# Performance work log

Hardware: AMD Instinct MI355X
Metric: run time of the kernel (lower is better)

The kernel has to match this reference:

```python
import jax, jax.numpy as jnp
import numpy as np

BASE = 257
HASH_MOD = 4096
WINDOWS = (2, 4, 8, 16)
MATCH_OFFSETS = (1, 2, 4, 8)
CHUNK = 32
EPS_LN = 1e-5


def _shift_right(x, k):
    # (B,T) -> shifted right by k along time, zero-filled
    B, T = x.shape
    return jnp.concatenate([jnp.zeros((B, k), x.dtype), x[:, :T - k]], axis=1)


def _rolling_hashes(chars):
    # polynomial rolling hash over each window size, mod HASH_MOD -> (B,T,S) int32
    c = chars.astype(jnp.int32)
    hs = []
    for w in WINDOWS:
        acc = jnp.zeros_like(c)
        p = 1
        for j in range(w):  # small fixed loop (<=16)
            acc = acc + _shift_right(c, j) * p
            p = (p * BASE) % HASH_MOD
        hs.append(acc % HASH_MOD)
    return jnp.stack(hs, axis=2)


def _match_features(chars):
    feats = []
    for k in MATCH_OFFSETS:
        m = (chars == _shift_right(chars, k)).astype(jnp.float32)
        m = m.at[:, :k].set(0.0)
        feats.append(m)
    return jnp.stack(feats, axis=-1)  # (B,T,n_match)


def _layer_norm(x, g, b):
    mu = jnp.mean(x, axis=-1, keepdims=True)
    var = jnp.mean((x - mu) ** 2, axis=-1, keepdims=True)
    return (x - mu) * jax.lax.rsqrt(var + EPS_LN) * g + b


def _forward(chars, emb_byte, hash_tables, Wq, bq, conv_w, conv_b, Win, b_in,
             Wg, bg, Wi, bi, Wo, bo, ln_g, ln_b, mlp_w, mlp_b, Wout, bout):
    B, T = chars.shape
    byte_emb = emb_byte[chars]                       # (B,T,Eb)
    hidx = _rolling_hashes(chars)                    # (B,T,S)
    scale_embeds = jnp.stack(
        [hash_tables[s][hidx[:, :, s]] for s in range(len(WINDOWS))], axis=2
    )                                                # (B,T,S,E)
    # scale attention: query from byte embedding, softmax over scales
    E = scale_embeds.shape[-1]
    q = byte_emb @ Wq + bq                           # (B,T,E)
    scores = jnp.einsum('bte,btse->bts', q, scale_embeds) / jnp.sqrt(jnp.float32(E))
    w = jax.nn.softmax(scores, axis=-1)
    hash_feat = jnp.einsum('bts,btse->bte', w, scale_embeds)
    # causal depthwise conv + silu
    C = hash_feat.shape[-1]
    kk = conv_w.shape[-1]
    ht = jnp.moveaxis(hash_feat, 1, 2)               # (B,C,T)
    ht = jnp.pad(ht, ((0, 0), (0, 0), (kk - 1, 0)))
    ht = jax.lax.conv_general_dilated(
        ht, conv_w, window_strides=(1,), padding='VALID',
        dimension_numbers=('NCH', 'OIH', 'NCH'), feature_group_count=C)
    hash_feat = jax.nn.silu(jnp.moveaxis(ht + conv_b[None, :, None], 2, 1))
    mf = _match_features(chars)
    feat = jnp.concatenate([byte_emb, hash_feat, mf], axis=-1)
    h = jax.nn.silu(feat @ Win + b_in)               # (B,T,H)
    # TinyScan: chunked log-space gated scan, carry across chunks via lax.scan
    gates = jax.nn.sigmoid(h @ Wg + bg)              # (B,T,S)
    drive = (1.0 - gates) * (h @ Wi + bi)
    S = gates.shape[-1]
    nC = T // CHUNK
    g = gates.reshape(B, nC, CHUNK, S).transpose(1, 0, 2, 3)
    d = drive.reshape(B, nC, CHUNK, S).transpose(1, 0, 2, 3)

    def step(hc, ab):
        a, b = ab                                    # (B,K,S)
        log_a = jnp.log(jnp.maximum(a, 1e-6))
        cum_a = jnp.exp(jnp.cumsum(log_a, axis=1))
        inv = 1.0 / jnp.maximum(cum_a, 1e-8)
        cum_wb = jnp.cumsum(b * inv, axis=1)
        out = cum_a * (hc[:, None, :] + cum_wb)
        return out[:, -1], out

    _, states = jax.lax.scan(step, jnp.zeros((B, S), h.dtype), (g, d))
    states = states.transpose(1, 0, 2, 3).reshape(B, T, S)
    h = _layer_norm(h + states @ Wo + bo, ln_g, ln_b)
    # residual MLP blocks: x + silu(Linear(x))
    for l in range(mlp_w.shape[0]):
        h = h + jax.nn.silu(h @ mlp_w[l] + mlp_b[l])
    return h @ Wout + bout                           # (B,T,V)


def setup_inputs() -> dict:
    key = jax.random.key(0)
    ks = jax.random.split(key, 12)
    B, T, V = 8, 8192, 256
    EB, E, H, SS, KC, NM, NR = 64, 64, 512, 32, 4, 4, 3
    feat = EB + E + NM

    def lin(k, i, o):
        return (jax.random.normal(k, (i, o), jnp.float32) / np.sqrt(i)).astype(jnp.float32)

    return {
        'chars': jax.random.randint(ks[0], (B, T), 0, V),
        'emb_byte': jax.random.normal(ks[1], (V, EB), jnp.float32) * 0.02,
        'hash_tables': jax.random.normal(ks[2], (len(WINDOWS), HASH_MOD, E), jnp.float32) * 0.02,
        'Wq': lin(ks[3], EB, E), 'bq': jnp.zeros((E,), jnp.float32),
        'conv_w': jax.random.normal(ks[4], (E, 1, KC), jnp.float32) * 0.2,
        'conv_b': jnp.zeros((E,), jnp.float32),
        'Win': lin(ks[5], feat, H), 'b_in': jnp.zeros((H,), jnp.float32),
        'Wg': lin(ks[6], H, SS), 'bg': jnp.zeros((SS,), jnp.float32),
        'Wi': lin(ks[7], H, SS), 'bi': jnp.zeros((SS,), jnp.float32),
        'Wo': lin(ks[8], SS, H), 'bo': jnp.zeros((H,), jnp.float32),
        'ln_g': jnp.ones((H,), jnp.float32), 'ln_b': jnp.zeros((H,), jnp.float32),
        'mlp_w': jax.random.normal(ks[9], (NR, H, H), jnp.float32) / np.sqrt(H),
        'mlp_b': jnp.zeros((NR, H), jnp.float32),
        'Wout': lin(ks[10], H, V), 'bout': jnp.zeros((V,), jnp.float32),
    }


def reference(chars, emb_byte, hash_tables, Wq, bq, conv_w, conv_b, Win, b_in,
              Wg, bg, Wi, bi, Wo, bo, ln_g, ln_b, mlp_w, mlp_b, Wout, bout):
    return _forward(chars, emb_byte, hash_tables, Wq, bq, conv_w, conv_b, Win, b_in,
                    Wg, bg, Wi, bi, Wo, bo, ln_g, ln_b, mlp_w, mlp_b, Wout, bout)
```

## Files before the change

kernel.cpp:

```cpp
#include <hip/hip_runtime.h>
#include <hip/hip_bf16.h>
#include <math.h>

#define B_ 8
#define T_ 8192
#define V_ 256
#define EB_ 64
#define E_ 64
#define H_ 512
#define SS_ 32
#define FEATP_ 160
#define NCH_ 256
#define CHUNK_ 32

typedef __attribute__((ext_vector_type(8))) short bf8;
typedef __attribute__((ext_vector_type(16))) float accv;

#define AS1(p) (__attribute__((address_space(1))) void*)(void*)(p)
#define AS3(p) (__attribute__((address_space(3))) void*)(void*)(p)

__device__ __forceinline__ float silu_f(float x) { return x / (1.0f + expf(-x)); }
__device__ __forceinline__ float sigm_f(float x) { return 1.0f / (1.0f + expf(-x)); }
__device__ __forceinline__ float bf2f(__hip_bfloat16 v) { return __bfloat162float(v); }
__device__ __forceinline__ __hip_bfloat16 f2bf(float v) { return __float2bfloat16(v); }
__device__ __forceinline__ float us2f(ushort u) {
    union { float f; unsigned int u32; } c; c.u32 = ((unsigned int)u) << 16; return c.f;
}
__device__ __forceinline__ ushort f2us(float v) {
    __hip_bfloat16 t = __float2bfloat16(v);
    return *reinterpret_cast<ushort*>(&t);
}

template <int KD>
__device__ __forceinline__ void mm128(const __hip_bfloat16* __restrict__ A,
                                      const __hip_bfloat16* __restrict__ Wt,
                                      int m0, int n0, accv (&acc)[2][2]) {
    __shared__ __align__(16) ushort lA[128 * 32];
    __shared__ __align__(16) ushort lB[128 * 32];
    int tid = threadIdx.x;
    int lane = tid & 63, w = tid >> 6;
    int wm = w & 1, wn = w >> 1;
    int c0 = w * 128 + lane;
    int c1 = c0 + 64;
    const ushort* Ab = (const ushort*)A;
    const ushort* Bb = (const ushort*)Wt;
    const ushort* gA0 = Ab + (size_t)(m0 + (c0 >> 2)) * KD + (c0 & 3) * 8;
    const ushort* gA1 = Ab + (size_t)(m0 + (c1 >> 2)) * KD + (c1 & 3) * 8;
    const ushort* gB0 = Bb + (size_t)(n0 + (c0 >> 2)) * KD + (c0 & 3) * 8;
    const ushort* gB1 = Bb + (size_t)(n0 + (c1 >> 2)) * KD + (c1 & 3) * 8;
    ushort* dA0 = &lA[(w * 128) * 8];
    ushort* dA1 = &lA[(w * 128 + 64) * 8];
    ushort* dB0 = &lB[(w * 128) * 8];
    ushort* dB1 = &lB[(w * 128 + 64) * 8];
    const ushort* pa = &lA[(64 * wm + (lane & 31)) * 32 + (lane >> 5) * 8];
    const ushort* pb = &lB[(64 * wn + (lane & 31)) * 32 + (lane >> 5) * 8];

    for (int kt = 0; kt < KD; kt += 32) {
        __builtin_amdgcn_global_load_lds(AS1(gA0 + kt), AS3(dA0), 16, 0, 0);
        __builtin_amdgcn_global_load_lds(AS1(gA1 + kt), AS3(dA1), 16, 0, 0);
        __builtin_amdgcn_global_load_lds(AS1(gB0 + kt), AS3(dB0), 16, 0, 0);
        __builtin_amdgcn_global_load_lds(AS1(gB1 + kt), AS3(dB1), 16, 0, 0);
        __syncthreads();
#pragma unroll
        for (int ks = 0; ks < 2; ks++) {
            bf8 a0 = *(const bf8*)(pa + ks * 16);
            bf8 a1 = *(const bf8*)(pa + 32 * 32 + ks * 16);
            bf8 b0 = *(const bf8*)(pb + ks * 16);
            bf8 b1 = *(const bf8*)(pb + 32 * 32 + ks * 16);
            acc[0][0] = __builtin_amdgcn_mfma_f32_32x32x16_bf16(a0, b0, acc[0][0], 0, 0, 0);
            acc[0][1] = __builtin_amdgcn_mfma_f32_32x32x16_bf16(a0, b1, acc[0][1], 0, 0, 0);
            acc[1][0] = __builtin_amdgcn_mfma_f32_32x32x16_bf16(a1, b0, acc[1][0], 0, 0, 0);
            acc[1][1] = __builtin_amdgcn_mfma_f32_32x32x16_bf16(a1, b1, acc[1][1], 0, 0, 0);
        }
        __syncthreads();
    }
}

__device__ __forceinline__ void zero_acc(accv (&acc)[2][2]) {
#pragma unroll
    for (int i = 0; i < 2; i++)
#pragma unroll
        for (int j = 0; j < 2; j++)
#pragma unroll
            for (int r = 0; r < 16; r++) acc[i][j][r] = 0.0f;
}

#define CD_ROW(r, lane) (((r) & 3) + 8 * ((r) >> 2) + 4 * ((lane) >> 5))

__global__ __launch_bounds__(256) void k_mlp_mfma(const __hip_bfloat16* __restrict__ hin,
                                                  const __hip_bfloat16* __restrict__ Wt,
                                                  const float* __restrict__ bias,
                                                  __hip_bfloat16* __restrict__ hout) {
    accv acc[2][2];
    zero_acc(acc);
    int lane = threadIdx.x & 63, w = threadIdx.x >> 6, wm = w & 1, wn = w >> 1;
    int m0 = blockIdx.x * 128, n0 = blockIdx.y * 128;
    mm128<H_>(hin, Wt, m0, n0, acc);
#pragma unroll
    for (int i = 0; i < 2; i++)
#pragma unroll
        for (int j = 0; j < 2; j++) {
            int col = n0 + 64 * wn + 32 * j + (lane & 31);
            float bv = bias[col];
#pragma unroll
            for (int r = 0; r < 16; r++) {
                int row = m0 + 64 * wm + 32 * i + CD_ROW(r, lane);
                float v = acc[i][j][r] + bv;
                float res = bf2f(hin[(size_t)row * H_ + col]);
                hout[(size_t)row * H_ + col] = f2bf(res + silu_f(v));
            }
        }
}

__global__ __launch_bounds__(256) void k_win_mfma(const __hip_bfloat16* __restrict__ featb,
                                                  const __hip_bfloat16* __restrict__ Wt,
                                                  const float* __restrict__ bias,
                                                  __hip_bfloat16* __restrict__ hb) {
    accv acc[2][2];
    zero_acc(acc);
    int lane = threadIdx.x & 63, w = threadIdx.x >> 6, wm = w & 1, wn = w >> 1;
    int m0 = blockIdx.x * 128, n0 = blockIdx.y * 128;
    mm128<FEATP_>(featb, Wt, m0, n0, acc);
#pragma unroll
    for (int i = 0; i < 2; i++)
#pragma unroll
        for (int j = 0; j < 2; j++) {
            int col = n0 + 64 * wn + 32 * j + (lane & 31);
            float bv = bias[col];
#pragma unroll
            for (int r = 0; r < 16; r++) {
                int row = m0 + 64 * wm + 32 * i + CD_ROW(r, lane);
                hb[(size_t)row * H_ + col] = f2bf(silu_f(acc[i][j][r] + bv));
            }
        }
}

__global__ __launch_bounds__(256) void k_womm(const __hip_bfloat16* __restrict__ states_bf,
                                              const __hip_bfloat16* __restrict__ Wt_wo,
                                              const float* __restrict__ bo,
                                              const __hip_bfloat16* __restrict__ hb,
                                              __hip_bfloat16* __restrict__ tmp) {
    accv acc[2][2];
    zero_acc(acc);
    int lane = threadIdx.x & 63, w = threadIdx.x >> 6, wm = w & 1, wn = w >> 1;
    int m0 = blockIdx.x * 128, n0 = blockIdx.y * 128;
    mm128<SS_>(states_bf, Wt_wo, m0, n0, acc);
#pragma unroll
    for (int i = 0; i < 2; i++)
#pragma unroll
        for (int j = 0; j < 2; j++) {
            int col = n0 + 64 * wn + 32 * j + (lane & 31);
            float bv = bo[col];
#pragma unroll
            for (int r = 0; r < 16; r++) {
                int row = m0 + 64 * wm + 32 * i + CD_ROW(r, lane);
                float res = bf2f(hb[(size_t)row * H_ + col]);
                tmp[(size_t)row * H_ + col] = f2bf(res + acc[i][j][r] + bv);
            }
        }
}

__global__ __launch_bounds__(256) void k_ln(const __hip_bfloat16* __restrict__ tmp,
                                            const float* __restrict__ ln_g,
                                            const float* __restrict__ ln_b,
                                            __hip_bfloat16* __restrict__ hb) {
    int wave = threadIdx.x >> 6, lane = threadIdx.x & 63;
    int token = blockIdx.x * 4 + wave;
    const ushort* row = (const ushort*)(tmp + (size_t)token * H_) + lane * 8;
    bf8 xv = *(const bf8*)row;
    float x[8];
    float sm = 0.f, sq = 0.f;
#pragma unroll
    for (int i = 0; i < 8; i++) {
        x[i] = us2f((ushort)xv[i]);
        sm += x[i];
        sq += x[i] * x[i];
    }
#pragma unroll
    for (int off = 32; off; off >>= 1) {
        sm += __shfl_xor(sm, off, 64);
        sq += __shfl_xor(sq, off, 64);
    }
    float mu = sm * (1.0f / 512.0f);
    float var = sq * (1.0f / 512.0f) - mu * mu;
    float rstd = rsqrtf(fmaxf(var, 0.0f) + 1e-5f);
    float4 g0 = *(const float4*)(ln_g + lane * 8);
    float4 g1 = *(const float4*)(ln_g + lane * 8 + 4);
    float4 b0 = *(const float4*)(ln_b + lane * 8);
    float4 b1 = *(const float4*)(ln_b + lane * 8 + 4);
    float gg[8] = {g0.x, g0.y, g0.z, g0.w, g1.x, g1.y, g1.z, g1.w};
    float bb[8] = {b0.x, b0.y, b0.z, b0.w, b1.x, b1.y, b1.z, b1.w};
    bf8 o;
#pragma unroll
    for (int i = 0; i < 8; i++) o[i] = (short)f2us((x[i] - mu) * rstd * gg[i] + bb[i]);
    *(bf8*)((ushort*)(hb + (size_t)token * H_) + lane * 8) = o;
}

__global__ __launch_bounds__(256) void k_out_mfma(const __hip_bfloat16* __restrict__ hb,
                                                  const __hip_bfloat16* __restrict__ Wt,
                                                  const float* __restrict__ bout,
                                                  float* __restrict__ out) {
    accv acc[2][2];
    zero_acc(acc);
    int lane = threadIdx.x & 63, w = threadIdx.x >> 6, wm = w & 1, wn = w >> 1;
    int m0 = blockIdx.x * 128, n0 = blockIdx.y * 128;
    mm128<H_>(hb, Wt, m0, n0, acc);
#pragma unroll
    for (int i = 0; i < 2; i++)
#pragma unroll
        for (int j = 0; j < 2; j++) {
            int col = n0 + 64 * wn + 32 * j + (lane & 31);
            float bv = bout[col];
#pragma unroll
            for (int r = 0; r < 16; r++) {
                int row = m0 + 64 * wm + 32 * i + CD_ROW(r, lane);
                out[(size_t)row * V_ + col] = acc[i][j][r] + bv;
            }
        }
}

__global__ __launch_bounds__(256) void k_gates_mfma(const __hip_bfloat16* __restrict__ hb,
                                                    const __hip_bfloat16* __restrict__ Wt_gd,
                                                    const float* __restrict__ bg,
                                                    const float* __restrict__ bi,
                                                    float* __restrict__ gates,
                                                    float* __restrict__ drive) {
    __shared__ __align__(16) ushort lA[256 * 32];
    __shared__ __align__(16) ushort lB[64 * 32];
    int tid = threadIdx.x, lane = tid & 63, w = tid >> 6;
    int m0 = blockIdx.x * 256;
    accv acc[2][2];
    zero_acc(acc);
    const ushort* Ab = (const ushort*)hb;
    const ushort* Bb = (const ushort*)Wt_gd;
    const ushort* pa = &lA[(64 * w + (lane & 31)) * 32 + (lane >> 5) * 8];
    const ushort* pb = &lB[((lane & 31)) * 32 + (lane >> 5) * 8];
    int cb = w * 64 + lane;
    const ushort* gB = Bb + (size_t)(cb >> 2) * H_ + (cb & 3) * 8;
    for (int kt = 0; kt < H_; kt += 32) {
#pragma unroll
        for (int j = 0; j < 4; j++) {
            int c = w * 256 + j * 64 + lane;
            __builtin_amdgcn_global_load_lds(
                AS1(Ab + (size_t)(m0 + (c >> 2)) * H_ + (c & 3) * 8 + kt),
                AS3(&lA[(w * 256 + j * 64) * 8]), 16, 0, 0);
        }
        __builtin_amdgcn_global_load_lds(AS1(gB + kt), AS3(&lB[(w * 64) * 8]), 16, 0, 0);
        __syncthreads();
#pragma unroll
        for (int ks = 0; ks < 2; ks++) {
            bf8 a0 = *(const bf8*)(pa + ks * 16);
            bf8 a1 = *(const bf8*)(pa + 32 * 32 + ks * 16);
            bf8 b0 = *(const bf8*)(pb + ks * 16);
            bf8 b1 = *(const bf8*)(pb + 32 * 32 + ks * 16);
            acc[0][0] = __builtin_amdgcn_mfma_f32_32x32x16_bf16(a0, b0, acc[0][0], 0, 0, 0);
            acc[0][1] = __builtin_amdgcn_mfma_f32_32x32x16_bf16(a0, b1, acc[0][1], 0, 0, 0);
            acc[1][0] = __builtin_amdgcn_mfma_f32_32x32x16_bf16(a1, b0, acc[1][0], 0, 0, 0);
            acc[1][1] = __builtin_amdgcn_mfma_f32_32x32x16_bf16(a1, b1, acc[1][1], 0, 0, 0);
        }
        __syncthreads();
    }
    int c = lane & 31;
    float bgv = bg[c], biv = bi[c];
#pragma unroll
    for (int i = 0; i < 2; i++)
#pragma unroll
        for (int r = 0; r < 16; r++) {
            int row = m0 + 64 * w + 32 * i + CD_ROW(r, lane);
            float g = sigm_f(acc[i][0][r] + bgv);
            float d = (1.0f - g) * (acc[i][1][r] + biv);
            gates[(size_t)row * SS_ + c] = g;
            drive[(size_t)row * SS_ + c] = d;
        }
}

__global__ __launch_bounds__(256) void k_prep_w(const float* __restrict__ mlp_w,
                                                const float* __restrict__ Wout,
                                                const float* __restrict__ Win,
                                                const float* __restrict__ Wg,
                                                const float* __restrict__ Wi,
                                                const float* __restrict__ Wo,
                                                const float* __restrict__ Wq,
                                                const float* __restrict__ bq,
                                                const float* __restrict__ emb_byte,
                                                __hip_bfloat16* __restrict__ Wt_mlp,
                                                __hip_bfloat16* __restrict__ Wt_out,
                                                __hip_bfloat16* __restrict__ Wt_win,
                                                __hip_bfloat16* __restrict__ Wt_gd,
                                                __hip_bfloat16* __restrict__ Wt_wo,
                                                float* __restrict__ Qtab) {
    int idx = blockIdx.x * 256 + threadIdx.x;
    if (idx < 786432) {
        int l = idx >> 18, rem = idx & 262143;
        int n = rem >> 9, k = rem & 511;
        Wt_mlp[idx] = f2bf(mlp_w[l * 262144 + k * 512 + n]);
    } else if (idx < 786432 + 131072) {
        int rem = idx - 786432;
        int n = rem >> 9, k = rem & 511;
        Wt_out[rem] = f2bf(Wout[k * 256 + n]);
    } else if (idx < 786432 + 131072 + 81920) {
        int rem = idx - (786432 + 131072);
        int n = rem / 160, k = rem % 160;
        Wt_win[rem] = f2bf(k < 132 ? Win[k * 512 + n] : 0.0f);
    } else if (idx < 786432 + 131072 + 81920 + 32768) {
        int rem = idx - (786432 + 131072 + 81920);
        int n = rem >> 9, k = rem & 511;
        Wt_gd[rem] = f2bf(n < 32 ? Wg[k * 32 + n] : Wi[k * 32 + (n - 32)]);
    } else if (idx < 786432 + 131072 + 81920 + 32768 + 16384) {
        int rem = idx - (786432 + 131072 + 81920 + 32768);
        int n = rem >> 5, k = rem & 31;
        Wt_wo[rem] = f2bf(Wo[k * H_ + n]);
    } else if (idx < 786432 + 131072 + 81920 + 32768 + 16384 + 16384) {
        int rem = idx - (786432 + 131072 + 81920 + 32768 + 16384);
        int c = rem >> 6, e = rem & 63;
        float a = bq[e];
#pragma unroll 8
        for (int k = 0; k < 64; k++) a += emb_byte[c * 64 + k] * Wq[k * 64 + e];
        Qtab[rem] = a * 0.125f;
    }
}

__global__ __launch_bounds__(256) void k_token_feats(
    const int* __restrict__ chars, const float* __restrict__ emb_byte,
    const float* __restrict__ hash_tables, const float* __restrict__ Qtab,
    __hip_bfloat16* __restrict__ featb, float* __restrict__ hfpre) {
    int wave = threadIdx.x >> 6, lane = threadIdx.x & 63;
    int token = blockIdx.x * 4 + wave;
    int t = token & (T_ - 1);
    int b = token >> 13;
    const int* crow = chars + b * T_;
    int cv[16];
#pragma unroll
    for (int j = 0; j < 16; j++) cv[j] = (t >= j) ? crow[t - j] : 0;
    int acc = 0;
    int hidx[4];
#pragma unroll
    for (int j = 0; j < 16; j++) {
        acc += cv[j] * (1 + 256 * j);
        if (j == 1) hidx[0] = acc & 4095;
        if (j == 3) hidx[1] = acc & 4095;
        if (j == 7) hidx[2] = acc & 4095;
        if (j == 15) hidx[3] = acc & 4095;
    }
    int c0 = cv[0];
    float be = emb_byte[c0 * EB_ + lane];
    float q = Qtab[c0 * 64 + lane];
    float se[4];
#pragma unroll
    for (int s = 0; s < 4; s++) se[s] = hash_tables[(s * 4096 + hidx[s]) * E_ + lane];
    float sc[4];
#pragma unroll
    for (int s = 0; s < 4; s++) {
        float v = q * se[s];
#pragma unroll
        for (int off = 32; off; off >>= 1) v += __shfl_xor(v, off, 64);
        sc[s] = v;
    }
    float mx = fmaxf(fmaxf(sc[0], sc[1]), fmaxf(sc[2], sc[3]));
    float w0 = expf(sc[0] - mx), w1 = expf(sc[1] - mx), w2 = expf(sc[2] - mx), w3 = expf(sc[3] - mx);
    float inv = 1.0f / (w0 + w1 + w2 + w3);
    float hf = (w0 * se[0] + w1 * se[1] + w2 * se[2] + w3 * se[3]) * inv;
    featb[(size_t)token * FEATP_ + lane] = f2bf(be);
    hfpre[(size_t)token * E_ + lane] = hf;
    if (lane < 32) {
        float m = 0.0f;
        if (lane < 4) {
            int k = 1 << lane;
            m = (t >= k && c0 == cv[k]) ? 1.0f : 0.0f;
        }
        featb[(size_t)token * FEATP_ + 128 + lane] = f2bf(m);
    }
}

__global__ __launch_bounds__(256) void k_conv(
    const float* __restrict__ hfpre, const float* __restrict__ conv_w,
    const float* __restrict__ conv_b, __hip_bfloat16* __restrict__ featb) {
    int idx = blockIdx.x * 256 + threadIdx.x;
    int e = idx & 63;
    int bt = idx >> 6;
    int t = bt & (T_ - 1);
    float acc = conv_b[e];
#pragma unroll
    for (int k = 0; k < 4; k++) {
        int tt = t - 3 + k;
        if (tt >= 0) acc += hfpre[(size_t)(bt - 3 + k) * E_ + e] * conv_w[e * 4 + k];
    }
    featb[(size_t)bt * FEATP_ + 64 + e] = f2bf(silu_f(acc));
}

__global__ __launch_bounds__(256) void k_chunk_ab(
    const float* __restrict__ gates, const float* __restrict__ drive,
    float* __restrict__ chA, float* __restrict__ chB) {
    int gid = blockIdx.x * 256 + threadIdx.x;
    int s = gid & 31;
    int n = (gid >> 5) & (NCH_ - 1);
    int b = gid >> 13;
    int base = (b * T_ + n * CHUNK_) * SS_ + s;
    float suml = 0.f, cum_wb = 0.f, cum_a = 1.f;
    for (int i = 0; i < CHUNK_; i++) {
        float g = gates[base + i * SS_];
        float d = drive[base + i * SS_];
        suml += logf(fmaxf(g, 1e-6f));
        cum_a = expf(suml);
        cum_wb += d / fmaxf(cum_a, 1e-8f);
    }
    chA[gid] = cum_a;
    chB[gid] = cum_a * cum_wb;
}

__global__ void k_chunk_scan(const float* __restrict__ chA, const float* __restrict__ chB,
                             float* __restrict__ chH) {
    int tid = threadIdx.x;
    int b = tid >> 5, s = tid & 31;
    const float* pA = chA + (size_t)b * NCH_ * SS_ + s;
    const float* pB = chB + (size_t)b * NCH_ * SS_ + s;
    float* pH = chH + (size_t)b * NCH_ * SS_ + s;
    float hc = 0.f;
    for (int n = 0; n < NCH_; n += 8) {
        float a[8], bb[8];
#pragma unroll
        for (int i = 0; i < 8; i++) {
            a[i] = pA[(n + i) * SS_];
            bb[i] = pB[(n + i) * SS_];
        }
#pragma unroll
        for (int i = 0; i < 8; i++) {
            pH[(n + i) * SS_] = hc;
            hc = a[i] * hc + bb[i];
        }
    }
}

__global__ __launch_bounds__(256) void k_states(
    const float* __restrict__ gates, const float* __restrict__ drive,
    const float* __restrict__ chH, __hip_bfloat16* __restrict__ states_bf) {
    int gid = blockIdx.x * 256 + threadIdx.x;
    int s = gid & 31;
    int n = (gid >> 5) & (NCH_ - 1);
    int b = gid >> 13;
    int base = (b * T_ + n * CHUNK_) * SS_ + s;
    float hc = chH[gid];
    float suml = 0.f, cum_wb = 0.f;
    for (int i = 0; i < CHUNK_; i++) {
        float g = gates[base + i * SS_];
        float d = drive[base + i * SS_];
        suml += logf(fmaxf(g, 1e-6f));
        float cum_a = expf(suml);
        cum_wb += d / fmaxf(cum_a, 1e-8f);
        states_bf[base + i * SS_] = f2bf(cum_a * (hc + cum_wb));
    }
}

extern "C" void kernel_launch(void* const* d_in, const int* in_sizes, int n_in,
                              void* d_out, int out_size, void* d_ws, size_t ws_size,
                              hipStream_t stream) {
    (void)in_sizes; (void)n_in; (void)out_size; (void)ws_size;
    const int*   chars       = (const int*)  d_in[0];
    const float* emb_byte    = (const float*)d_in[1];
    const float* hash_tables = (const float*)d_in[2];
    const float* Wq          = (const float*)d_in[3];
    const float* bq          = (const float*)d_in[4];
    const float* conv_w      = (const float*)d_in[5];
    const float* conv_b      = (const float*)d_in[6];
    const float* Win         = (const float*)d_in[7];
    const float* b_in        = (const float*)d_in[8];
    const float* Wg          = (const float*)d_in[9];
    const float* bg          = (const float*)d_in[10];
    const float* Wi          = (const float*)d_in[11];
    const float* bi          = (const float*)d_in[12];
    const float* Wo          = (const float*)d_in[13];
    const float* bo          = (const float*)d_in[14];
    const float* ln_g        = (const float*)d_in[15];
    const float* ln_b        = (const float*)d_in[16];
    const float* mlp_w       = (const float*)d_in[17];
    const float* mlp_b       = (const float*)d_in[18];
    const float* Wout        = (const float*)d_in[19];
    const float* bout        = (const float*)d_in[20];
    float* out = (float*)d_out;

    const size_t NTOK = (size_t)B_ * T_;
    char* p = (char*)d_ws;
    auto alloc = [&](size_t bytes) { void* r = (void*)p; p += (bytes + 255) & ~(size_t)255; return r; };
    __hip_bfloat16* featb = (__hip_bfloat16*)alloc(NTOK * FEATP_ * 2);
    float*          hfpre = (float*)alloc(NTOK * E_ * 4);
    __hip_bfloat16* hbA   = (__hip_bfloat16*)alloc(NTOK * H_ * 2);
    __hip_bfloat16* hbB   = (__hip_bfloat16*)alloc(NTOK * H_ * 2);
    float*          gates = (float*)alloc(NTOK * SS_ * 4);
    float*          drive = (float*)alloc(NTOK * SS_ * 4);
    __hip_bfloat16* states_bf = (__hip_bfloat16*)alloc(NTOK * SS_ * 2);
    float*          chA   = (float*)alloc((size_t)B_ * NCH_ * SS_ * 4);
    float*          chB   = (float*)alloc((size_t)B_ * NCH_ * SS_ * 4);
    float*          chH   = (float*)alloc((size_t)B_ * NCH_ * SS_ * 4);
    __hip_bfloat16* Wt_mlp= (__hip_bfloat16*)alloc(3 * 512 * 512 * 2);
    __hip_bfloat16* Wt_out= (__hip_bfloat16*)alloc(256 * 512 * 2);
    __hip_bfloat16* Wt_win= (__hip_bfloat16*)alloc(512 * FEATP_ * 2);
    __hip_bfloat16* Wt_gd = (__hip_bfloat16*)alloc(64 * 512 * 2);
    __hip_bfloat16* Wt_wo = (__hip_bfloat16*)alloc(512 * SS_ * 2);
    float*          Qtab  = (float*)alloc(256 * 64 * 4);

    k_prep_w<<<4160, 256, 0, stream>>>(mlp_w, Wout, Win, Wg, Wi, Wo, Wq, bq, emb_byte,
                                       Wt_mlp, Wt_out, Wt_win, Wt_gd, Wt_wo, Qtab);
    k_token_feats<<<NTOK / 4, 256, 0, stream>>>(chars, emb_byte, hash_tables, Qtab, featb, hfpre);
    k_conv<<<NTOK * E_ / 256, 256, 0, stream>>>(hfpre, conv_w, conv_b, featb);
    k_win_mfma<<<dim3(NTOK / 128, 4), 256, 0, stream>>>(featb, Wt_win, b_in, hbA);
    k_gates_mfma<<<NTOK / 256, 256, 0, stream>>>(hbA, Wt_gd, bg, bi, gates, drive);
    k_chunk_ab<<<B_ * NCH_ * SS_ / 256, 256, 0, stream>>>(gates, drive, chA, chB);
    k_chunk_scan<<<1, 256, 0, stream>>>(chA, chB, chH);
    k_states<<<B_ * NCH_ * SS_ / 256, 256, 0, stream>>>(gates, drive, chH, states_bf);
    k_womm<<<dim3(NTOK / 128, 4), 256, 0, stream>>>(states_bf, Wt_wo, bo, hbA, hbB);
    k_ln<<<NTOK / 4, 256, 0, stream>>>(hbB, ln_g, ln_b, hbA);
    k_mlp_mfma<<<dim3(NTOK / 128, 4), 256, 0, stream>>>(hbA, Wt_mlp, mlp_b, hbB);
    k_mlp_mfma<<<dim3(NTOK / 128, 4), 256, 0, stream>>>(hbB, Wt_mlp + 262144, mlp_b + 512, hbA);
    k_mlp_mfma<<<dim3(NTOK / 128, 4), 256, 0, stream>>>(hbA, Wt_mlp + 524288, mlp_b + 1024, hbB);
    k_out_mfma<<<dim3(NTOK / 128, 2), 256, 0, stream>>>(hbB, Wt_out, bout, out);
}
```

Measured before the change: 546.3 us.

## Replace 128x128 MFMA GEMMs with pipelined 256x256-tile kernels using direct-to-LDS loads

Adds a new GEMM core, mm256, that gives each 512-thread block a 256x256 output tile. It double-buffers K-slices in LDS through global_load_lds, with staged waitcnt/barrier steps, s_setprio around the MFMA bursts, and an XCD-aware block swizzle. The Win, MLP and output projections switch to this core. To fit the 64-wide K steps, the feature matrix padding grows from 160 to 192 columns, with the extra columns zero-filled. The aim is more operand reuse per LDS byte and overlap of global loads with MFMA work, at the cost of about 128KB of LDS per block, which leaves one resident block per CU and lower occupancy.

```diff
diff --git a/kernel.cpp b/kernel.cpp
--- a/kernel.cpp
+++ b/kernel.cpp
@@ -9,7 +9,7 @@
 #define E_ 64
 #define H_ 512
 #define SS_ 32
-#define FEATP_ 160
+#define FEATP_ 192
 #define NCH_ 256
 #define CHUNK_ 32
 
@@ -29,6 +29,174 @@
 __device__ __forceinline__ ushort f2us(float v) {
     __hip_bfloat16 t = __float2bfloat16(v);
     return *reinterpret_cast<ushort*>(&t);
+}
+
+#define CD_ROW(r, lane) (((r) & 3) + 8 * ((r) >> 2) + 4 * ((lane) >> 5))
+
+__device__ __forceinline__ int xcd_swz(int bid, int nwg) {
+    return (bid & 7) * (nwg >> 3) + (bid >> 3);
+}
+
+template <int KD>
+__device__ __forceinline__ void mm256(const ushort* __restrict__ Ab,
+                                      const ushort* __restrict__ Bb,
+                                      int m0, int n0, accv (&acc)[4][2]) {
+    constexpr int NT = KD / 64;
+    __shared__ __align__(1024) ushort lA[32768];
+    __shared__ __align__(1024) ushort lB[32768];
+    const int tid  = threadIdx.x;
+    const int lane = tid & 63;
+    const int w    = tid >> 6;
+    const int wm   = w >> 2, wn = w & 3;
+
+    const int srow = tid & 255;
+    const int sh   = tid >> 8;
+    const ushort* gA = Ab + (size_t)(m0 + srow) * KD + sh * 8;
+    const ushort* gB = Bb + (size_t)(n0 + srow) * KD + sh * 8;
+    const int doff  = w * 512;
+    const int raoff = (lane >> 5) * 2048 + (128 * wm + (lane & 31)) * 8;
+    const int rboff = (lane >> 5) * 2048 + (64 * wn + (lane & 31)) * 8;
+
+#define STG(slot, f, koff)                                                                          \
+    do {                                                                                            \
+        __builtin_amdgcn_global_load_lds(AS1(gA + (koff) + (f) * 16),                               \
+                                         AS3(&lA[(slot) * 16384 + (f) * 4096 + doff]), 16, 0, 0);   \
+        __builtin_amdgcn_global_load_lds(AS1(gB + (koff) + (f) * 16),                               \
+                                         AS3(&lB[(slot) * 16384 + (f) * 4096 + doff]), 16, 0, 0);   \
+    } while (0)
+
+#define WAITBAR(n)                                                    \
+    do {                                                              \
+        asm volatile("s_waitcnt vmcnt(" #n ")" ::: "memory");         \
+        __builtin_amdgcn_s_barrier();                                 \
+        __builtin_amdgcn_sched_barrier(0);                            \
+    } while (0)
+
+#define PH(slot, f)                                                                                \
+    do {                                                                                           \
+        const ushort* pa = &lA[(slot) * 16384 + (f) * 4096 + raoff];                               \
+        const ushort* pb = &lB[(slot) * 16384 + (f) * 4096 + rboff];                               \
+        bf8 b0v = *(const bf8*)(pb);                                                               \
+        bf8 b1v = *(const bf8*)(pb + 256);                                                         \
+        bf8 a0v = *(const bf8*)(pa);                                                               \
+        bf8 a1v = *(const bf8*)(pa + 256);                                                         \
+        bf8 a2v = *(const bf8*)(pa + 512);                                                         \
+        bf8 a3v = *(const bf8*)(pa + 768);                                                         \
+        __builtin_amdgcn_s_setprio(1);                                                             \
+        acc[0][0] = __builtin_amdgcn_mfma_f32_32x32x16_bf16(a0v, b0v, acc[0][0], 0, 0, 0);         \
+        acc[0][1] = __builtin_amdgcn_mfma_f32_32x32x16_bf16(a0v, b1v, acc[0][1], 0, 0, 0);         \
+        acc[1][0] = __builtin_amdgcn_mfma_f32_32x32x16_bf16(a1v, b0v, acc[1][0], 0, 0, 0);         \
+        acc[1][1] = __builtin_amdgcn_mfma_f32_32x32x16_bf16(a1v, b1v, acc[1][1], 0, 0, 0);         \
+        acc[2][0] = __builtin_amdgcn_mfma_f32_32x32x16_bf16(a2v, b0v, acc[2][0], 0, 0, 0);         \
+        acc[2][1] = __builtin_amdgcn_mfma_f32_32x32x16_bf16(a2v, b1v, acc[2][1], 0, 0, 0);         \
+        acc[3][0] = __builtin_amdgcn_mfma_f32_32x32x16_bf16(a3v, b0v, acc[3][0], 0, 0, 0);         \
+        acc[3][1] = __builtin_amdgcn_mfma_f32_32x32x16_bf16(a3v, b1v, acc[3][1], 0, 0, 0);         \
+        __builtin_amdgcn_s_setprio(0);                                                             \
+    } while (0)
+
+    STG(0, 0, 0); STG(0, 1, 0); STG(0, 2, 0); STG(0, 3, 0);
+    int kt = 64;
+    for (int t = 0; t < NT - 1; ++t) {
+        const int slot = t & 1;
+        STG(slot ^ 1, 0, kt); WAITBAR(8); PH(slot, 0);
+        STG(slot ^ 1, 1, kt); WAITBAR(8); PH(slot, 1);
+        STG(slot ^ 1, 2, kt); WAITBAR(8); PH(slot, 2);
+        STG(slot ^ 1, 3, kt); WAITBAR(8); PH(slot, 3);
+        kt += 64;
+    }
+    {
+        const int ls = (NT - 1) & 1;
+        WAITBAR(6); PH(ls, 0);
+        WAITBAR(4); PH(ls, 1);
+        WAITBAR(2); PH(ls, 2);
+        WAITBAR(0); PH(ls, 3);
+    }
+#undef STG
+#undef WAITBAR
+#undef PH
+}
+
+__device__ __forceinline__ void zero_acc8(accv (&acc)[4][2]) {
+#pragma unroll
+    for (int i = 0; i < 4; i++)
+#pragma unroll
+        for (int j = 0; j < 2; j++)
+#pragma unroll
+            for (int r = 0; r < 16; r++) acc[i][j][r] = 0.0f;
+}
+
+__global__ __launch_bounds__(512, 2) void k_mlp256(const __hip_bfloat16* __restrict__ hin,
+                                                   const __hip_bfloat16* __restrict__ Wt,
+                                                   const float* __restrict__ bias,
+                                                   __hip_bfloat16* __restrict__ hout) {
+    accv acc[4][2];
+    zero_acc8(acc);
+    int wg = xcd_swz(blockIdx.x, 512);
+    int m0 = (wg >> 1) * 256, n0 = (wg & 1) * 256;
+    int lane = threadIdx.x & 63, w = threadIdx.x >> 6, wm = w >> 2, wn = w & 3;
+    mm256<H_>((const ushort*)hin, (const ushort*)Wt, m0, n0, acc);
+#pragma unroll
+    for (int fr = 0; fr < 4; fr++)
+#pragma unroll
+        for (int fc = 0; fc < 2; fc++) {
+            int col = n0 + 64 * wn + 32 * fc + (lane & 31);
+            float bv = bias[col];
+#pragma unroll
+            for (int r = 0; r < 16; r++) {
+                int row = m0 + 128 * wm + 32 * fr + CD_ROW(r, lane);
+                float v = acc[fr][fc][r] + bv;
+                float res = bf2f(hin[(size_t)row * H_ + col]);
+                hout[(size_t)row * H_ + col] = f2bf(res + silu_f(v));
+            }
+        }
+}
+
+__global__ __launch_bounds__(512, 2) void k_win256(const __hip_bfloat16* __restrict__ featb,
+                                                   const __hip_bfloat16* __restrict__ Wt,
+                                                   const float* __restrict__ bias,
+                                                   __hip_bfloat16* __restrict__ hb) {
+    accv acc[4][2];
+    zero_acc8(acc);
+    int wg = xcd_swz(blockIdx.x, 512);
+    int m0 = (wg >> 1) * 256, n0 = (wg & 1) * 256;
+    int lane = threadIdx.x & 63, w = threadIdx.x >> 6, wm = w >> 2, wn = w & 3;
+    mm256<FEATP_>((const ushort*)featb, (const ushort*)Wt, m0, n0, acc);
+#pragma unroll
+    for (int fr = 0; fr < 4; fr++)
+#pragma unroll
+        for (int fc = 0; fc < 2; fc++) {
+            int col = n0 + 64 * wn + 32 * fc + (lane & 31);
+            float bv = bias[col];
+#pragma unroll
+            for (int r = 0; r < 16; r++) {
+                int row = m0 + 128 * wm + 32 * fr + CD_ROW(r, lane);
+                hb[(size_t)row * H_ + col] = f2bf(silu_f(acc[fr][fc][r] + bv));
+            }
+        }
+}
+
+__global__ __launch_bounds__(512, 2) void k_out256(const __hip_bfloat16* __restrict__ hb,
+                                                   const __hip_bfloat16* __restrict__ Wt,
+                                                   const float* __restrict__ bout,
+                                                   float* __restrict__ out) {
+    accv acc[4][2];
+    zero_acc8(acc);
+    int wg = xcd_swz(blockIdx.x, 256);
+    int m0 = wg * 256;
+    int lane = threadIdx.x & 63, w = threadIdx.x >> 6, wm = w >> 2, wn = w & 3;
+    mm256<H_>((const ushort*)hb, (const ushort*)Wt, m0, 0, acc);
+#pragma unroll
+    for (int fr = 0; fr < 4; fr++)
+#pragma unroll
+        for (int fc = 0; fc < 2; fc++) {
+            int col = 64 * wn + 32 * fc + (lane & 31);
+            float bv = bout[col];
+#pragma unroll
+            for (int r = 0; r < 16; r++) {
+                int row = m0 + 128 * wm + 32 * fr + CD_ROW(r, lane);
+                out[(size_t)row * V_ + col] = acc[fr][fc][r] + bv;
+            }
+        }
 }
 
 template <int KD>
@@ -85,56 +253,6 @@
             for (int r = 0; r < 16; r++) acc[i][j][r] = 0.0f;
 }
 
-#define CD_ROW(r, lane) (((r) & 3) + 8 * ((r) >> 2) + 4 * ((lane) >> 5))
-
-__global__ __launch_bounds__(256) void k_mlp_mfma(const __hip_bfloat16* __restrict__ hin,
-                                                  const __hip_bfloat16* __restrict__ Wt,
-                                                  const float* __restrict__ bias,
-                                                  __hip_bfloat16* __restrict__ hout) {
-    accv acc[2][2];
-    zero_acc(acc);
-    int lane = threadIdx.x & 63, w = threadIdx.x >> 6, wm = w & 1, wn = w >> 1;
-    int m0 = blockIdx.x * 128, n0 = blockIdx.y * 128;
-    mm128<H_>(hin, Wt, m0, n0, acc);
-#pragma unroll
-    for (int i = 0; i < 2; i++)
-#pragma unroll
-        for (int j = 0; j < 2; j++) {
-            int col = n0 + 64 * wn + 32 * j + (lane & 31);
-            float bv = bias[col];
-#pragma unroll
-            for (int r = 0; r < 16; r++) {
-                int row = m0 + 64 * wm + 32 * i + CD_ROW(r, lane);
-                float v = acc[i][j][r] + bv;
-                float res = bf2f(hin[(size_t)row * H_ + col]);
-                hout[(size_t)row * H_ + col] = f2bf(res + silu_f(v));
-            }
-        }
-}
-
-__global__ __launch_bounds__(256) void k_win_mfma(const __hip_bfloat16* __restrict__ featb,
-                                                  const __hip_bfloat16* __restrict__ Wt,
-                                                  const float* __restrict__ bias,
-                                                  __hip_bfloat16* __restrict__ hb) {
-    accv acc[2][2];
-    zero_acc(acc);
-    int lane = threadIdx.x & 63, w = threadIdx.x >> 6, wm = w & 1, wn = w >> 1;
-    int m0 = blockIdx.x * 128, n0 = blockIdx.y * 128;
-    mm128<FEATP_>(featb, Wt, m0, n0, acc);
-#pragma unroll
-    for (int i = 0; i < 2; i++)
-#pragma unroll
-        for (int j = 0; j < 2; j++) {
-            int col = n0 + 64 * wn + 32 * j + (lane & 31);
-            float bv = bias[col];
-#pragma unroll
-            for (int r = 0; r < 16; r++) {
-                int row = m0 + 64 * wm + 32 * i + CD_ROW(r, lane);
-                hb[(size_t)row * H_ + col] = f2bf(silu_f(acc[i][j][r] + bv));
-            }
-        }
-}
-
 __global__ __launch_bounds__(256) void k_womm(const __hip_bfloat16* __restrict__ states_bf,
                                               const __hip_bfloat16* __restrict__ Wt_wo,
                                               const float* __restrict__ bo,
@@ -194,29 +312,6 @@
 #pragma unroll
     for (int i = 0; i < 8; i++) o[i] = (short)f2us((x[i] - mu) * rstd * gg[i] + bb[i]);
     *(bf8*)((ushort*)(hb + (size_t)token * H_) + lane * 8) = o;
-}
-
-__global__ __launch_bounds__(256) void k_out_mfma(const __hip_bfloat16* __restrict__ hb,
-                                                  const __hip_bfloat16* __restrict__ Wt,
-                                                  const float* __restrict__ bout,
-                                                  float* __restrict__ out) {
-    accv acc[2][2];
-    zero_acc(acc);
-    int lane = threadIdx.x & 63, w = threadIdx.x >> 6, wm = w & 1, wn = w >> 1;
-    int m0 = blockIdx.x * 128, n0 = blockIdx.y * 128;
-    mm128<H_>(hb, Wt, m0, n0, acc);
-#pragma unroll
-    for (int i = 0; i < 2; i++)
-#pragma unroll
-        for (int j = 0; j < 2; j++) {
-            int col = n0 + 64 * wn + 32 * j + (lane & 31);
-            float bv = bout[col];
-#pragma unroll
-            for (int r = 0; r < 16; r++) {
-                int row = m0 + 64 * wm + 32 * i + CD_ROW(r, lane);
-                out[(size_t)row * V_ + col] = acc[i][j][r] + bv;
-            }
-        }
 }
 
 __global__ __launch_bounds__(256) void k_gates_mfma(const __hip_bfloat16* __restrict__ hb,
@@ -294,24 +389,24 @@
         int l = idx >> 18, rem = idx & 262143;
         int n = rem >> 9, k = rem & 511;
         Wt_mlp[idx] = f2bf(mlp_w[l * 262144 + k * 512 + n]);
-    } else if (idx < 786432 + 131072) {
+    } else if (idx < 917504) {
         int rem = idx - 786432;
         int n = rem >> 9, k = rem & 511;
         Wt_out[rem] = f2bf(Wout[k * 256 + n]);
-    } else if (idx < 786432 + 131072 + 81920) {
-        int rem = idx - (786432 + 131072);
-        int n = rem / 160, k = rem % 160;
+    } else if (idx < 1015808) {
+        int rem = idx - 917504;
+        int n = rem / FEATP_, k = rem % FEATP_;
         Wt_win[rem] = f2bf(k < 132 ? Win[k * 512 + n] : 0.0f);
-    } else if (idx < 786432 + 131072 + 81920 + 32768) {
-        int rem = idx - (786432 + 131072 + 81920);
+    } else if (idx < 1048576) {
+        int rem = idx - 1015808;
         int n = rem >> 9, k = rem & 511;
         Wt_gd[rem] = f2bf(n < 32 ? Wg[k * 32 + n] : Wi[k * 32 + (n - 32)]);
-    } else if (idx < 786432 + 131072 + 81920 + 32768 + 16384) {
-        int rem = idx - (786432 + 131072 + 81920 + 32768);
+    } else if (idx < 1064960) {
+        int rem = idx - 1048576;
         int n = rem >> 5, k = rem & 31;
         Wt_wo[rem] = f2bf(Wo[k * H_ + n]);
-    } else if (idx < 786432 + 131072 + 81920 + 32768 + 16384 + 16384) {
-        int rem = idx - (786432 + 131072 + 81920 + 32768 + 16384);
+    } else if (idx < 1081344) {
+        int rem = idx - 1064960;
         int c = rem >> 6, e = rem & 63;
         float a = bq[e];
 #pragma unroll 8
@@ -369,6 +464,8 @@
             m = (t >= k && c0 == cv[k]) ? 1.0f : 0.0f;
         }
         featb[(size_t)token * FEATP_ + 128 + lane] = f2bf(m);
+    } else {
+        featb[(size_t)token * FEATP_ + 128 + lane] = f2bf(0.0f);
     }
 }
 
@@ -498,19 +595,19 @@
     __hip_bfloat16* Wt_wo = (__hip_bfloat16*)alloc(512 * SS_ * 2);
     float*          Qtab  = (float*)alloc(256 * 64 * 4);
 
-    k_prep_w<<<4160, 256, 0, stream>>>(mlp_w, Wout, Win, Wg, Wi, Wo, Wq, bq, emb_byte,
+    k_prep_w<<<4224, 256, 0, stream>>>(mlp_w, Wout, Win, Wg, Wi, Wo, Wq, bq, emb_byte,
                                        Wt_mlp, Wt_out, Wt_win, Wt_gd, Wt_wo, Qtab);
     k_token_feats<<<NTOK / 4, 256, 0, stream>>>(chars, emb_byte, hash_tables, Qtab, featb, hfpre);
     k_conv<<<NTOK * E_ / 256, 256, 0, stream>>>(hfpre, conv_w, conv_b, featb);
-    k_win_mfma<<<dim3(NTOK / 128, 4), 256, 0, stream>>>(featb, Wt_win, b_in, hbA);
+    k_win256<<<512, 512, 0, stream>>>(featb, Wt_win, b_in, hbA);
     k_gates_mfma<<<NTOK / 256, 256, 0, stream>>>(hbA, Wt_gd, bg, bi, gates, drive);
     k_chunk_ab<<<B_ * NCH_ * SS_ / 256, 256, 0, stream>>>(gates, drive, chA, chB);
     k_chunk_scan<<<1, 256, 0, stream>>>(chA, chB, chH);
     k_states<<<B_ * NCH_ * SS_ / 256, 256, 0, stream>>>(gates, drive, chH, states_bf);
     k_womm<<<dim3(NTOK / 128, 4), 256, 0, stream>>>(states_bf, Wt_wo, bo, hbA, hbB);
     k_ln<<<NTOK / 4, 256, 0, stream>>>(hbB, ln_g, ln_b, hbA);
-    k_mlp_mfma<<<dim3(NTOK / 128, 4), 256, 0, stream>>>(hbA, Wt_mlp, mlp_b, hbB);
-    k_mlp_mfma<<<dim3(NTOK / 128, 4), 256, 0, stream>>>(hbB, Wt_mlp + 262144, mlp_b + 512, hbA);
-    k_mlp_mfma<<<dim3(NTOK / 128, 4), 256, 0, stream>>>(hbA, Wt_mlp + 524288, mlp_b + 1024, hbB);
-    k_out_mfma<<<dim3(NTOK / 128, 2), 256, 0, stream>>>(hbB, Wt_out, bout, out);
-}
+    k_mlp256<<<512, 512, 0, stream>>>(hbA, Wt_mlp, mlp_b, hbB);
+    k_mlp256<<<512, 512, 0, stream>>>(hbB, Wt_mlp + 262144, mlp_b + 512, hbA);
+    k_mlp256<<<512, 512, 0, stream>>>(hbA, Wt_mlp + 524288, mlp_b + 1024, hbB);
+    k_out256<<<256, 512, 0, stream>>>(hbB, Wt_out, bout, out);
+}
```

After: 645.4 us. +18.1%, slower.
